# Optimization experiments

Hardware: AMD Instinct MI355X
Metric: run time of the kernel (lower is better)

The kernel has to match this reference:

```python
import jax, jax.numpy as jnp
import numpy as np

D_MODEL = 2048
NUM_HEADS = 16
HEAD_DIM = 128
ROPE_BASE = 10000.0
NEG_INF = -1e9


def setup_inputs() -> dict:
    key = jax.random.key(0)
    ks = jax.random.split(key, 5)
    B, S = 2, 2048
    hidden_states = jax.random.normal(ks[0], (B, S, D_MODEL), dtype=jnp.float32)
    # additive causal mask: 0 on/below diagonal, large-negative above
    causal = jnp.triu(jnp.full((S, S), NEG_INF, dtype=jnp.float32), k=1)
    attention_mask = jnp.broadcast_to(causal, (B, 1, S, S))
    position_ids = jnp.broadcast_to(jnp.arange(S, dtype=jnp.int32), (B, S))
    scale = 1.0 / np.sqrt(D_MODEL)
    Wq = jax.random.normal(ks[1], (D_MODEL, NUM_HEADS * HEAD_DIM), dtype=jnp.float32) * scale
    Wk = jax.random.normal(ks[2], (D_MODEL, NUM_HEADS * HEAD_DIM), dtype=jnp.float32) * scale
    Wv = jax.random.normal(ks[3], (D_MODEL, NUM_HEADS * HEAD_DIM), dtype=jnp.float32) * scale
    Wo = jax.random.normal(ks[4], (NUM_HEADS * HEAD_DIM, D_MODEL), dtype=jnp.float32) * scale
    return {"hidden_states": hidden_states, "attention_mask": attention_mask,
            "position_ids": position_ids, "Wq": Wq, "Wk": Wk, "Wv": Wv, "Wo": Wo}


def _rope_cos_sin(position_ids):
    # inv_freq: [head_dim/2]
    inv_freq = 1.0 / (ROPE_BASE ** (jnp.arange(0, HEAD_DIM, 2, dtype=jnp.float32) / HEAD_DIM))
    freqs = position_ids.astype(jnp.float32)[..., None] * inv_freq  # [B,S,hd/2]
    emb = jnp.concatenate([freqs, freqs], axis=-1)  # [B,S,hd]
    return jnp.cos(emb), jnp.sin(emb)


def _rotate_half(x):
    x1, x2 = jnp.split(x, 2, axis=-1)
    return jnp.concatenate([-x2, x1], axis=-1)


def reference(hidden_states, attention_mask, position_ids, Wq, Wk, Wv, Wo):
    B, S, _ = hidden_states.shape
    H, Dh = NUM_HEADS, HEAD_DIM
    q = (hidden_states @ Wq).reshape(B, S, H, Dh).transpose(0, 2, 1, 3)  # [B,H,S,Dh]
    k = (hidden_states @ Wk).reshape(B, S, H, Dh).transpose(0, 2, 1, 3)
    v = (hidden_states @ Wv).reshape(B, S, H, Dh).transpose(0, 2, 1, 3)
    cos, sin = _rope_cos_sin(position_ids)  # [B,S,Dh]
    cos = cos[:, None, :, :]  # [B,1,S,Dh]
    sin = sin[:, None, :, :]
    q = q * cos + _rotate_half(q) * sin
    k = k * cos + _rotate_half(k) * sin
    scaling = 1.0 / np.sqrt(Dh)
    scores = jnp.einsum('bhqd,bhkd->bhqk', q, k) * scaling  # [B,H,S,S]
    scores = scores + attention_mask[:, :, :, :S]
    attn = jax.nn.softmax(scores.astype(jnp.float32), axis=-1).astype(q.dtype)
    # dropout p=0.0 / eval mode -> identity
    out = jnp.einsum('bhqk,bhkd->bhqd', attn, v)  # [B,H,S,Dh]
    out = out.transpose(0, 2, 1, 3).reshape(B, S, H * Dh)
    return out @ Wo
```

## Files before the change

kernel.cpp:

```cpp
#include <hip/hip_runtime.h>

typedef __attribute__((ext_vector_type(4))) float f32x4;
typedef __attribute__((ext_vector_type(8))) _Float16 f16x8;
typedef __attribute__((ext_vector_type(4))) _Float16 f16x4;

#define SEQ 2048
#define DM 2048
#define NQKV 6144

__device__ __forceinline__ void gload16(const _Float16* g, _Float16* l) {
  __builtin_amdgcn_global_load_lds(
      (const __attribute__((address_space(1))) void*)g,
      (__attribute__((address_space(3))) void*)l, 16, 0, 0);
}

__global__ __launch_bounds__(256) void cvt_x_kernel(const float* __restrict__ X,
                                                    _Float16* __restrict__ Xb, int n4) {
  int i = blockIdx.x * 256 + threadIdx.x;
  if (i < n4) {
    const float4 v = ((const float4*)X)[i];
    f16x4 o;
    o.x = (_Float16)v.x; o.y = (_Float16)v.y; o.z = (_Float16)v.z; o.w = (_Float16)v.w;
    ((f16x4*)Xb)[i] = o;
  }
}

__global__ __launch_bounds__(256) void wtrans_all_kernel(const float* __restrict__ Wq,
                                                         const float* __restrict__ Wk,
                                                         const float* __restrict__ Wv,
                                                         const float* __restrict__ Wo,
                                                         _Float16* __restrict__ Wqkvt,
                                                         _Float16* __restrict__ Wot) {
  __shared__ float tile[32][33];
  const int z = blockIdx.z;
  const float* W = (z == 0) ? Wq : (z == 1) ? Wk : (z == 2) ? Wv : Wo;
  _Float16* Wt = (z < 3) ? (Wqkvt + (size_t)z * 2048 * 2048) : Wot;
  const int n0 = blockIdx.x * 32, k0 = blockIdx.y * 32;
  const int tx = threadIdx.x & 31, ty = threadIdx.x >> 5;
#pragma unroll
  for (int i = 0; i < 32; i += 8)
    tile[ty + i][tx] = W[(size_t)(k0 + ty + i) * 2048 + n0 + tx];
  __syncthreads();
#pragma unroll
  for (int i = 0; i < 32; i += 8)
    Wt[(size_t)(n0 + ty + i) * 2048 + k0 + tx] = (_Float16)tile[tx][ty + i];
}

__global__ __launch_bounds__(256) void rope_table_kernel(float* __restrict__ ct,
                                                         float* __restrict__ st) {
  int i = blockIdx.x * 256 + threadIdx.x;
  int pos = i >> 6, f = i & 63;
  float inv = powf(10000.0f, -(float)f / 64.0f);
  float ang = (float)pos * inv;
  ct[i] = cosf(ang);
  st[i] = sinf(ang);
}

template <int MODE>
__global__ __launch_bounds__(512, 2) void gemm8n_kernel(
    const _Float16* __restrict__ A, const _Float16* __restrict__ Bt,
    float* __restrict__ Cout, int M, int N, int K,
    const int* __restrict__ pos_ids, const float* __restrict__ ct,
    const float* __restrict__ st, _Float16* __restrict__ Qo,
    _Float16* __restrict__ Ko, _Float16* __restrict__ Vo) {
  __shared__ __align__(16) char smem[147456];
  _Float16* As = (_Float16*)smem;
  _Float16* Bs = (_Float16*)(smem + 98304);
  const int nwg = gridDim.x * gridDim.y;
  const int orig = blockIdx.y * gridDim.x + blockIdx.x;
  const int id = (orig & 7) * (nwg >> 3) + (orig >> 3);
  const int bx = id % gridDim.x, by = id / gridDim.x;
  const int bm = by * 256, bn = bx * 128;
  const int t = threadIdx.x, lane = t & 63, w = t >> 6;
  const int wm = w >> 2, wn = w & 3;
  const int rl = lane & 15, lr4 = lane >> 4;
  const int NKT = K >> 6;

  const int srow = t >> 3;
  const int scol = ((t & 7) ^ (srow & 7)) << 3;
  const _Float16* pA = A + (size_t)(bm + srow) * K + scol;
  const _Float16* pB = Bt + (size_t)(bn + srow) * K + scol;
  _Float16* lA = As + t * 8;
  _Float16* lB = Bs + t * 8;
  const size_t rowK64 = (size_t)64 * K;

#define STA(H, KT, SLOT)                                                   \
  { const size_t _g = (size_t)((H) * 128) * K + (size_t)(KT) * 64;         \
    gload16(pA + _g, lA + (SLOT) * 16384 + (H) * 8192);                    \
    gload16(pA + _g + rowK64, lA + (SLOT) * 16384 + (H) * 8192 + 4096); }
#define STB(KT, SLOT)                                                      \
  { const size_t _g = (size_t)(KT) * 64;                                   \
    gload16(pB + _g, lB + (SLOT) * 8192);                                  \
    gload16(pB + _g + rowK64, lB + (SLOT) * 8192 + 4096); }

  const int sw0 = (lr4 ^ (rl & 7)) << 3;
  const int sw1 = ((4 + lr4) ^ (rl & 7)) << 3;
  const int aoff = (wm * 64 + rl) * 64;
  const int boff = (wn * 32 + rl) * 64;

  f16x8 a_[4][2], b_[2][2];
  f32x4 acc[2][4][2];
#pragma unroll
  for (int qm = 0; qm < 2; ++qm)
#pragma unroll
    for (int mf = 0; mf < 4; ++mf)
#pragma unroll
      for (int nf = 0; nf < 2; ++nf) acc[qm][mf][nf] = (f32x4)0.0f;

#define LOAD_A(H, SLOT)                                                 \
  { const _Float16* _p = As + (SLOT) * 16384 + (H) * 8192 + aoff;       \
    _Pragma("unroll") for (int mf = 0; mf < 4; ++mf) {                  \
      a_[mf][0] = *(const f16x8*)&_p[mf * 1024 + sw0];                  \
      a_[mf][1] = *(const f16x8*)&_p[mf * 1024 + sw1]; } }
#define LOAD_B(SLOT)                                                    \
  { const _Float16* _p = Bs + (SLOT) * 8192 + boff;                     \
    _Pragma("unroll") for (int nf = 0; nf < 2; ++nf) {                  \
      b_[nf][0] = *(const f16x8*)&_p[nf * 1024 + sw0];                  \
      b_[nf][1] = *(const f16x8*)&_p[nf * 1024 + sw1]; } }
#define MFMA_Q(QM)                                                      \
  __builtin_amdgcn_s_setprio(1);                                        \
  _Pragma("unroll") for (int mf = 0; mf < 4; ++mf)                      \
    _Pragma("unroll") for (int nf = 0; nf < 2; ++nf) {                  \
      acc[QM][mf][nf] = __builtin_amdgcn_mfma_f32_16x16x32_f16(         \
          a_[mf][0], b_[nf][0], acc[QM][mf][nf], 0, 0, 0);              \
      acc[QM][mf][nf] = __builtin_amdgcn_mfma_f32_16x16x32_f16(         \
          a_[mf][1], b_[nf][1], acc[QM][mf][nf], 0, 0, 0); }            \
  __builtin_amdgcn_s_setprio(0);
#define BAR()                                                           \
  do { __builtin_amdgcn_sched_barrier(0); __builtin_amdgcn_s_barrier(); \
       __builtin_amdgcn_sched_barrier(0); } while (0)
#define LGKM0()                                                         \
  do { asm volatile("s_waitcnt lgkmcnt(0)" ::: "memory");               \
       __builtin_amdgcn_sched_barrier(0); } while (0)
#define VM6() asm volatile("s_waitcnt vmcnt(6)" ::: "memory")
#define VM0() asm volatile("s_waitcnt vmcnt(0)" ::: "memory")

  STA(0, 0, 0); STB(0, 0); STA(1, 0, 0);
  STA(0, 1, 1); STB(1, 1); STA(1, 1, 1);
  VM6();
  BAR();

  for (int jb = 0; jb + 4 < NKT; jb += 3) {
    LOAD_A(0, 0); LOAD_B(0); STA(0, jb + 2, 2); STB(jb + 2, 2);
    BAR(); LGKM0(); MFMA_Q(0); BAR();
    LOAD_A(1, 0); STA(1, jb + 2, 2);
    VM6(); BAR(); LGKM0(); MFMA_Q(1); BAR();
    LOAD_A(0, 1); LOAD_B(1); STA(0, jb + 3, 0); STB(jb + 3, 0);
    BAR(); LGKM0(); MFMA_Q(0); BAR();
    LOAD_A(1, 1); STA(1, jb + 3, 0);
    VM6(); BAR(); LGKM0(); MFMA_Q(1); BAR();
    LOAD_A(0, 2); LOAD_B(2); STA(0, jb + 4, 1); STB(jb + 4, 1);
    BAR(); LGKM0(); MFMA_Q(0); BAR();
    LOAD_A(1, 2); STA(1, jb + 4, 1);
    VM6(); BAR(); LGKM0(); MFMA_Q(1); BAR();
  }
  {
    LOAD_A(0, 0); LOAD_B(0);
    BAR(); LGKM0(); MFMA_Q(0); BAR();
    LOAD_A(1, 0);
    VM0();
    BAR(); LGKM0(); MFMA_Q(1); BAR();
    LOAD_A(0, 1); LOAD_B(1);
    BAR(); LGKM0(); MFMA_Q(0); BAR();
    LOAD_A(1, 1);
    BAR(); LGKM0(); MFMA_Q(1);
  }

  if (MODE == 0) {
#pragma unroll
    for (int qm = 0; qm < 2; ++qm)
#pragma unroll
      for (int mf = 0; mf < 4; ++mf)
#pragma unroll
        for (int nf = 0; nf < 2; ++nf) {
          const int col = bn + wn * 32 + nf * 16 + rl;
#pragma unroll
          for (int ri = 0; ri < 4; ++ri) {
            const int row = bm + qm * 128 + wm * 64 + mf * 16 + lr4 * 4 + ri;
            Cout[(size_t)row * N + col] = acc[qm][mf][nf][ri];
          }
        }
  } else {
    const int ttype = bx >> 4;
    const int hh = bx & 15;
    if (ttype == 2) {
#pragma unroll
      for (int qm = 0; qm < 2; ++qm)
#pragma unroll
        for (int mf = 0; mf < 4; ++mf)
#pragma unroll
          for (int nf = 0; nf < 2; ++nf) {
            const int d = wn * 32 + nf * 16 + rl;
            const int s0 = bm + qm * 128 + wm * 64 + mf * 16 + lr4 * 4;
            const int bb = s0 >> 11, ss = s0 & 2047;
            f16x4 v4;
#pragma unroll
            for (int ri = 0; ri < 4; ++ri) v4[ri] = (_Float16)acc[qm][mf][nf][ri];
            *(f16x4*)&Vo[((size_t)(bb * 16 + hh) * 128 + d) * SEQ + ss] = v4;
          }
    } else {
      float* cl = (float*)smem;
      LGKM0();
      BAR();
#pragma unroll
      for (int qm = 0; qm < 2; ++qm)
#pragma unroll
        for (int mf = 0; mf < 4; ++mf)
#pragma unroll
          for (int nf = 0; nf < 2; ++nf) {
            const int col = wn * 32 + nf * 16 + rl;
            const int r0 = qm * 128 + wm * 64 + mf * 16 + lr4 * 4;
#pragma unroll
            for (int ri = 0; ri < 4; ++ri) cl[(r0 + ri) * 130 + col] = acc[qm][mf][nf][ri];
          }
      BAR();
      const int row = t >> 1, pb = (t & 1) * 32;
      const int rg = bm + row;
      const int bb = rg >> 11, ss = rg & 2047;
      const int pos = pos_ids[rg];
      const float* cp = ct + pos * 64 + pb;
      const float* sp = st + pos * 64 + pb;
      _Float16* dst = (ttype ? Ko : Qo) + ((size_t)(bb * 16 + hh) * SEQ + ss) * 128;
      const float qs = ttype ? 1.0f : 0.08838834764831845f;
      const float* crow = cl + row * 130;
      _Float16 o1[32], o2[32];
#pragma unroll
      for (int i = 0; i < 32; ++i) {
        const float x1 = crow[pb + i], x2 = crow[pb + 64 + i];
        const float c = cp[i], s = sp[i];
        o1[i] = (_Float16)((x1 * c - x2 * s) * qs);
        o2[i] = (_Float16)((x2 * c + x1 * s) * qs);
      }
#pragma unroll
      for (int i = 0; i < 4; ++i) {
        *(f16x8*)&dst[pb + i * 8] = *(f16x8*)&o1[i * 8];
        *(f16x8*)&dst[pb + 64 + i * 8] = *(f16x8*)&o2[i * 8];
      }
    }
  }
#undef STA
#undef STB
#undef LOAD_A
#undef LOAD_B
#undef MFMA_Q
#undef BAR
#undef LGKM0
#undef VM6
#undef VM0
}

__global__ __launch_bounds__(512) void attn_kernel(const _Float16* __restrict__ Q,
                                                   const _Float16* __restrict__ K,
                                                   const _Float16* __restrict__ Vt,
                                                   _Float16* __restrict__ O) {
  __shared__ __align__(16) _Float16 Ks[2][64 * 128];
  __shared__ __align__(16) _Float16 Vs[2][128 * 64];
  __shared__ __align__(16) _Float16 Ps[8][16 * 72];
  const int bh = blockIdx.x;
  const int pair = blockIdx.y;
  const int b = bh >> 4, h = bh & 15;
  const int t = threadIdx.x, lane = t & 63, w = t >> 6;
  const int lr = lane >> 4, lc = lane & 15;
  const _Float16* Qb = Q + (size_t)bh * SEQ * 128;
  const _Float16* Kb = K + (size_t)bh * SEQ * 128;
  const _Float16* Vb = Vt + (size_t)bh * 128 * SEQ;

  auto stage = [&](int buf, int kb) {
    const int k0 = kb * 64;
#pragma unroll
    for (int i = 0; i < 2; ++i) {
      const int c = i * 512 + t;
      const int row = c >> 4, u = c & 15;
      gload16(&Kb[(size_t)(k0 + row) * 128 + ((u ^ (row & 7)) * 8)], &Ks[buf][c * 8]);
    }
#pragma unroll
    for (int i = 0; i < 2; ++i) {
      const int c = i * 512 + t;
      const int dim = c >> 3, u = c & 7;
      gload16(&Vb[(size_t)dim * SEQ + k0 + ((u ^ (dim & 7)) * 8)], &Vs[buf][c * 8]);
    }
  };

  for (int half = 0; half < 2; ++half) {
    const int j = half ? (15 - pair) : pair;
    const int q0 = j * 128;
    const int nkb = 2 * j + 2;
    const int rowmin = q0 + w * 16;

    f16x8 qf[4];
    {
      const int qrow = q0 + w * 16 + lc;
#pragma unroll
      for (int kk = 0; kk < 4; ++kk)
        qf[kk] = *(const f16x8*)&Qb[(size_t)qrow * 128 + kk * 32 + lr * 8];
    }
    f32x4 acco[8];
#pragma unroll
    for (int i = 0; i < 8; ++i) acco[i] = (f32x4)0.0f;
    float m_r[4] = {-1e30f, -1e30f, -1e30f, -1e30f};
    float l_r[4] = {0.f, 0.f, 0.f, 0.f};

    stage(0, 0);
    __syncthreads();
    for (int kb = 0; kb < nkb; ++kb) {
      const int cur = kb & 1;
      if (kb + 1 < nkb) stage(cur ^ 1, kb + 1);
      const int k0 = kb * 64;
      if (k0 <= rowmin + 15) {
        f32x4 sacc[4];
#pragma unroll
        for (int jj = 0; jj < 4; ++jj) sacc[jj] = (f32x4)0.0f;
#pragma unroll
        for (int jj = 0; jj < 4; ++jj) {
          const int krow = jj * 16 + lc;
#pragma unroll
          for (int kk = 0; kk < 4; ++kk) {
            const int idx = (krow * 128 + kk * 32 + lr * 8) ^ ((krow & 7) << 3);
            f16x8 kf = *(const f16x8*)&Ks[cur][idx];
            sacc[jj] = __builtin_amdgcn_mfma_f32_16x16x32_f16(qf[kk], kf, sacc[jj], 0, 0, 0);
          }
        }
        const bool diag = (k0 + 63 > rowmin);
#pragma unroll
        for (int r = 0; r < 4; ++r) {
          const int rowi = rowmin + lr * 4 + r;
          float s[4], mx = -1e30f;
#pragma unroll
          for (int jj = 0; jj < 4; ++jj) {
            float sv = sacc[jj][r];
            if (diag && (k0 + jj * 16 + lc > rowi)) sv = -1e30f;
            s[jj] = sv;
            mx = fmaxf(mx, sv);
          }
#pragma unroll
          for (int msk = 1; msk < 16; msk <<= 1) mx = fmaxf(mx, __shfl_xor(mx, msk));
          const float mn = fmaxf(m_r[r], mx);
          const float sc = __expf(m_r[r] - mn);
          float rs = 0.f;
#pragma unroll
          for (int jj = 0; jj < 4; ++jj) {
            float pv = __expf(s[jj] - mn);
            rs += pv;
            Ps[w][(lr * 4 + r) * 72 + jj * 16 + lc] = (_Float16)pv;
          }
#pragma unroll
          for (int msk = 1; msk < 16; msk <<= 1) rs += __shfl_xor(rs, msk);
          l_r[r] = l_r[r] * sc + rs;
          m_r[r] = mn;
#pragma unroll
          for (int tt = 0; tt < 8; ++tt) acco[tt][r] *= sc;
        }
#pragma unroll
        for (int tt = 0; tt < 8; ++tt) {
          const int dim = tt * 16 + lc;
#pragma unroll
          for (int ch = 0; ch < 2; ++ch) {
            f16x8 pf = *(const f16x8*)&Ps[w][lc * 72 + ch * 32 + lr * 8];
            const int vidx = (dim * 64 + ch * 32 + lr * 8) ^ ((dim & 7) << 3);
            f16x8 vf = *(const f16x8*)&Vs[cur][vidx];
            acco[tt] = __builtin_amdgcn_mfma_f32_16x16x32_f16(pf, vf, acco[tt], 0, 0, 0);
          }
        }
      }
      __syncthreads();
    }
#pragma unroll
    for (int tt = 0; tt < 8; ++tt) {
      const int col = h * 128 + tt * 16 + lc;
#pragma unroll
      for (int r = 0; r < 4; ++r) {
        const int row = q0 + w * 16 + lr * 4 + r;
        O[(size_t)(b * SEQ + row) * DM + col] = (_Float16)(acco[tt][r] / l_r[r]);
      }
    }
  }
}

extern "C" void kernel_launch(void* const* d_in, const int* in_sizes, int n_in,
                              void* d_out, int out_size, void* d_ws, size_t ws_size,
                              hipStream_t stream) {
  const float* hidden = (const float*)d_in[0];
  const int* pos_ids = (const int*)d_in[2];
  const float* Wq = (const float*)d_in[3];
  const float* Wk = (const float*)d_in[4];
  const float* Wv = (const float*)d_in[5];
  const float* Wo = (const float*)d_in[6];

  char* ws = (char*)d_ws;
  _Float16* Xb    = (_Float16*)(ws + 0);
  _Float16* Wqkvt = (_Float16*)(ws + 16777216);
  _Float16* Wot   = (_Float16*)(ws + 41943040);
  _Float16* Qbuf  = (_Float16*)(ws + 50331648);
  _Float16* Kbuf  = (_Float16*)(ws + 67108864);
  _Float16* Vtbuf = (_Float16*)(ws + 83886080);
  _Float16* Obuf  = (_Float16*)(ws + 100663296);
  float* ct       = (float*)(ws + 117440512);
  float* st       = (float*)(ws + 117964800);

  cvt_x_kernel<<<8192, 256, 0, stream>>>(hidden, Xb, 2097152);
  wtrans_all_kernel<<<dim3(64, 64, 4), 256, 0, stream>>>(Wq, Wk, Wv, Wo, Wqkvt, Wot);
  rope_table_kernel<<<512, 256, 0, stream>>>(ct, st);

  gemm8n_kernel<1><<<dim3(48, 16), 512, 0, stream>>>(
      Xb, Wqkvt, nullptr, 4096, 6144, 2048, pos_ids, ct, st, Qbuf, Kbuf, Vtbuf);

  attn_kernel<<<dim3(32, 8), 512, 0, stream>>>(Qbuf, Kbuf, Vtbuf, Obuf);

  gemm8n_kernel<0><<<dim3(16, 16), 512, 0, stream>>>(
      Obuf, Wot, (float*)d_out, 4096, 2048, 2048, nullptr, nullptr, nullptr,
      nullptr, nullptr, nullptr);
}
```

Measured before the change: 281.7 us.

## Vectorize weight transpose and overlap K/V prefetch with explicit waitcnt barriers

```diff
diff --git a/kernel.cpp b/kernel.cpp
--- a/kernel.cpp
+++ b/kernel.cpp
@@ -31,19 +31,27 @@
                                                          const float* __restrict__ Wo,
                                                          _Float16* __restrict__ Wqkvt,
                                                          _Float16* __restrict__ Wot) {
-  __shared__ float tile[32][33];
+  __shared__ float tile[64][65];
   const int z = blockIdx.z;
   const float* W = (z == 0) ? Wq : (z == 1) ? Wk : (z == 2) ? Wv : Wo;
   _Float16* Wt = (z < 3) ? (Wqkvt + (size_t)z * 2048 * 2048) : Wot;
-  const int n0 = blockIdx.x * 32, k0 = blockIdx.y * 32;
-  const int tx = threadIdx.x & 31, ty = threadIdx.x >> 5;
-#pragma unroll
-  for (int i = 0; i < 32; i += 8)
-    tile[ty + i][tx] = W[(size_t)(k0 + ty + i) * 2048 + n0 + tx];
+  const int n0 = blockIdx.x * 64, k0 = blockIdx.y * 64;
+  const int tx = threadIdx.x & 15, ty = threadIdx.x >> 4;
+#pragma unroll
+  for (int i = 0; i < 4; ++i) {
+    const int r = ty + i * 16;
+    const float4 v = *(const float4*)&W[(size_t)(k0 + r) * 2048 + n0 + tx * 4];
+    tile[r][tx * 4] = v.x; tile[r][tx * 4 + 1] = v.y;
+    tile[r][tx * 4 + 2] = v.z; tile[r][tx * 4 + 3] = v.w;
+  }
   __syncthreads();
-#pragma unroll
-  for (int i = 0; i < 32; i += 8)
-    Wt[(size_t)(n0 + ty + i) * 2048 + k0 + tx] = (_Float16)tile[tx][ty + i];
+  const int r = threadIdx.x >> 2, u = threadIdx.x & 3;
+  _Float16 o[16];
+#pragma unroll
+  for (int i = 0; i < 16; ++i) o[i] = (_Float16)tile[u * 16 + i][r];
+  _Float16* dst = &Wt[(size_t)(n0 + r) * 2048 + k0 + u * 16];
+  *(f16x8*)&dst[0] = *(f16x8*)&o[0];
+  *(f16x8*)&dst[8] = *(f16x8*)&o[8];
 }
 
 __global__ __launch_bounds__(256) void rope_table_kernel(float* __restrict__ ct,
@@ -265,6 +273,14 @@
   const _Float16* Kb = K + (size_t)bh * SEQ * 128;
   const _Float16* Vb = Vt + (size_t)bh * 128 * SEQ;
 
+  f16x8 onef;
+#pragma unroll
+  for (int i = 0; i < 8; ++i) onef[i] = (_Float16)1.0f;
+
+#define ABAR()                                                          \
+  do { __builtin_amdgcn_sched_barrier(0); __builtin_amdgcn_s_barrier(); \
+       __builtin_amdgcn_sched_barrier(0); } while (0)
+
   auto stage = [&](int buf, int kb) {
     const int k0 = kb * 64;
 #pragma unroll
@@ -301,10 +317,16 @@
     float l_r[4] = {0.f, 0.f, 0.f, 0.f};
 
     stage(0, 0);
-    __syncthreads();
     for (int kb = 0; kb < nkb; ++kb) {
       const int cur = kb & 1;
-      if (kb + 1 < nkb) stage(cur ^ 1, kb + 1);
+      const bool more = kb + 1 < nkb;
+      if (more) {
+        stage(cur ^ 1, kb + 1);
+        asm volatile("s_waitcnt vmcnt(4)" ::: "memory");
+      } else {
+        asm volatile("s_waitcnt vmcnt(0)" ::: "memory");
+      }
+      ABAR();
       const int k0 = kb * 64;
       if (k0 <= rowmin + 15) {
         f32x4 sacc[4];
@@ -336,33 +358,35 @@
           for (int msk = 1; msk < 16; msk <<= 1) mx = fmaxf(mx, __shfl_xor(mx, msk));
           const float mn = fmaxf(m_r[r], mx);
           const float sc = __expf(m_r[r] - mn);
-          float rs = 0.f;
 #pragma unroll
           for (int jj = 0; jj < 4; ++jj) {
-            float pv = __expf(s[jj] - mn);
-            rs += pv;
+            const float pv = __expf(s[jj] - mn);
             Ps[w][(lr * 4 + r) * 72 + jj * 16 + lc] = (_Float16)pv;
           }
-#pragma unroll
-          for (int msk = 1; msk < 16; msk <<= 1) rs += __shfl_xor(rs, msk);
-          l_r[r] = l_r[r] * sc + rs;
+          l_r[r] *= sc;
           m_r[r] = mn;
 #pragma unroll
           for (int tt = 0; tt < 8; ++tt) acco[tt][r] *= sc;
         }
+        f16x8 pf0 = *(const f16x8*)&Ps[w][lc * 72 + lr * 8];
+        f16x8 pf1 = *(const f16x8*)&Ps[w][lc * 72 + 32 + lr * 8];
+        f32x4 psum = (f32x4)0.0f;
+        psum = __builtin_amdgcn_mfma_f32_16x16x32_f16(pf0, onef, psum, 0, 0, 0);
+        psum = __builtin_amdgcn_mfma_f32_16x16x32_f16(pf1, onef, psum, 0, 0, 0);
 #pragma unroll
         for (int tt = 0; tt < 8; ++tt) {
           const int dim = tt * 16 + lc;
-#pragma unroll
-          for (int ch = 0; ch < 2; ++ch) {
-            f16x8 pf = *(const f16x8*)&Ps[w][lc * 72 + ch * 32 + lr * 8];
-            const int vidx = (dim * 64 + ch * 32 + lr * 8) ^ ((dim & 7) << 3);
-            f16x8 vf = *(const f16x8*)&Vs[cur][vidx];
-            acco[tt] = __builtin_amdgcn_mfma_f32_16x16x32_f16(pf, vf, acco[tt], 0, 0, 0);
-          }
+          const int v0 = (dim * 64 + lr * 8) ^ ((dim & 7) << 3);
+          const int v1 = (dim * 64 + 32 + lr * 8) ^ ((dim & 7) << 3);
+          acco[tt] = __builtin_amdgcn_mfma_f32_16x16x32_f16(
+              pf0, *(const f16x8*)&Vs[cur][v0], acco[tt], 0, 0, 0);
+          acco[tt] = __builtin_amdgcn_mfma_f32_16x16x32_f16(
+              pf1, *(const f16x8*)&Vs[cur][v1], acco[tt], 0, 0, 0);
         }
+#pragma unroll
+        for (int r = 0; r < 4; ++r) l_r[r] += psum[r];
       }
-      __syncthreads();
+      ABAR();
     }
 #pragma unroll
     for (int tt = 0; tt < 8; ++tt) {
@@ -374,6 +398,7 @@
       }
     }
   }
+#undef ABAR
 }
 
 extern "C" void kernel_launch(void* const* d_in, const int* in_sizes, int n_in,
@@ -398,7 +423,7 @@
   float* st       = (float*)(ws + 117964800);
 
   cvt_x_kernel<<<8192, 256, 0, stream>>>(hidden, Xb, 2097152);
-  wtrans_all_kernel<<<dim3(64, 64, 4), 256, 0, stream>>>(Wq, Wk, Wv, Wo, Wqkvt, Wot);
+  wtrans_all_kernel<<<dim3(32, 32, 4), 256, 0, stream>>>(Wq, Wk, Wv, Wo, Wqkvt, Wot);
   rope_table_kernel<<<512, 256, 0, stream>>>(ct, st);
 
   gemm8n_kernel<1><<<dim3(48, 16), 512, 0, stream>>>(
```

New measurement: 275.5 us. 2.2% less time.
